# Kernel tuning notes

Measured on AMD Instinct MI355X. Metric: run time of the kernel, lower is better.

The kernel has to match this reference:

```python
import jax, jax.numpy as jnp
import numpy as np


def setup_inputs() -> dict:
    key = jax.random.key(0)
    k1, k2, k3 = jax.random.split(key, 3)
    N, M, H = 32768, 4096, 768
    fact = jax.random.normal(k1, (N, H), dtype=jnp.float32)
    elements_p = jax.random.normal(k2, (M, H), dtype=jnp.float32)
    # kaiming_uniform with a=sqrt(5) on [H,H]: bound = sqrt(6/((1+5)*H)) = 1/sqrt(H)
    bound = 1.0 / np.sqrt(H)
    weights = jax.random.uniform(k3, (H, H), dtype=jnp.float32, minval=-bound, maxval=bound)
    return {"fact": fact, "elements_p": elements_p, "weights": weights}


def reference(fact, elements_p, weights):
    # fact: [N,H], elements_p: [M,H], weights: [H,H]
    fact_Q = jnp.max(fact, axis=0, keepdims=True)                 # [1,H]
    f2e = (fact_Q @ weights) @ elements_p.T                        # [1,M]
    f2e = jax.nn.softmax(f2e, axis=-1)
    elements_p_ = jnp.sum(elements_p * f2e.T, axis=0, keepdims=True)  # [1,H]
    e2f = (fact @ weights) @ elements_p_.T                         # [N,1]
    e2f = jax.nn.softmax(e2f, axis=0)
    fact_ = jnp.sum(fact * e2f, axis=0, keepdims=True)             # [1,H]
    return (fact_, elements_p_)
```

## Files before the change

### kernel.cpp

```cpp
#include <hip/hip_runtime.h>
#include <math.h>


#define H 768
#define H4 192
#define PSTRIDE 772
#define ACC_OFF 4
#define NBLK 256
#define NQ 48
#define NCOL 192

__device__ __forceinline__ float wave_max(float x) {
#pragma unroll
  for (int o = 32; o; o >>= 1) x = fmaxf(x, __shfl_xor(x, o, 64));
  return x;
}
__device__ __forceinline__ float wave_sum(float x) {
#pragma unroll
  for (int o = 32; o; o >>= 1) x += __shfl_xor(x, o, 64);
  return x;
}
__device__ __forceinline__ float4 f4max(float4 a, float4 b) {
  return make_float4(fmaxf(a.x, b.x), fmaxf(a.y, b.y), fmaxf(a.z, b.z), fmaxf(a.w, b.w));
}

struct SMem {
  float4 sacc[8][H4];
  float sred[16];
};

__device__ __forceinline__ void stream_pass(const float4* __restrict__ X4,
                                            const float* __restrict__ wvec,
                                            float* __restrict__ part, int R,
                                            SMem& sm) {
  const int tid = threadIdx.x, lane = tid & 63, wv = tid >> 6;
  float4 wr[3];
#pragma unroll
  for (int j = 0; j < 3; ++j) wr[j] = ((const float4*)wvec)[lane + 64 * j];
  const int nw = NBLK * 8;
  const int gw = blockIdx.x * 8 + wv;
  const int rpw = (R + nw - 1) / nw;
  const int r0 = gw * rpw;
  const int r1 = min(R, r0 + rpw);
  float mrun = -INFINITY, l = 0.f;
  float4 acc[3];
#pragma unroll
  for (int j = 0; j < 3; ++j) acc[j] = make_float4(0.f, 0.f, 0.f, 0.f);
  for (int r = r0; r < r1; ++r) {
    const float4* row = X4 + (size_t)r * H4;
    float4 x[3];
    float s = 0.f;
#pragma unroll
    for (int j = 0; j < 3; ++j) {
      x[j] = row[lane + 64 * j];
      s = fmaf(x[j].x, wr[j].x, s);
      s = fmaf(x[j].y, wr[j].y, s);
      s = fmaf(x[j].z, wr[j].z, s);
      s = fmaf(x[j].w, wr[j].w, s);
    }
    s = wave_sum(s);
    const float mn = fmaxf(mrun, s);
    const float esc = __expf(mrun - mn);
    const float p = __expf(s - mn);
    l = fmaf(l, esc, p);
#pragma unroll
    for (int j = 0; j < 3; ++j) {
      acc[j].x = fmaf(acc[j].x, esc, p * x[j].x);
      acc[j].y = fmaf(acc[j].y, esc, p * x[j].y);
      acc[j].z = fmaf(acc[j].z, esc, p * x[j].z);
      acc[j].w = fmaf(acc[j].w, esc, p * x[j].w);
    }
    mrun = mn;
  }
  if (lane == 0) { sm.sred[wv] = mrun; sm.sred[8 + wv] = l; }
#pragma unroll
  for (int j = 0; j < 3; ++j) sm.sacc[wv][lane + 64 * j] = acc[j];
  __syncthreads();
  if (wv == 0) {
    float gm = -INFINITY;
#pragma unroll
    for (int w2 = 0; w2 < 8; ++w2) gm = fmaxf(gm, sm.sred[w2]);
    float fa[8];
    float L = 0.f;
#pragma unroll
    for (int w2 = 0; w2 < 8; ++w2) {
      const float lw = sm.sred[8 + w2];
      fa[w2] = (lw > 0.f) ? __expf(sm.sred[w2] - gm) : 0.f;
      L = fmaf(fa[w2], lw, L);
    }
    float* pb = part + (size_t)blockIdx.x * PSTRIDE;
#pragma unroll
    for (int j = 0; j < 3; ++j) {
      float4 a = make_float4(0.f, 0.f, 0.f, 0.f);
#pragma unroll
      for (int w2 = 0; w2 < 8; ++w2) {
        const float4 t = sm.sacc[w2][lane + 64 * j];
        a.x = fmaf(fa[w2], t.x, a.x);
        a.y = fmaf(fa[w2], t.y, a.y);
        a.z = fmaf(fa[w2], t.z, a.z);
        a.w = fmaf(fa[w2], t.w, a.w);
      }
      *(float4*)(pb + ACC_OFF + 4 * (lane + 64 * j)) = a;
    }
    if (lane == 0) { pb[0] = gm; pb[1] = L; }
  }
}

__global__ __launch_bounds__(192) void k_colmax(const float4* __restrict__ x4,
                                                float4* __restrict__ pmax4, int N,
                                                unsigned int* __restrict__ cnts,
                                                float* __restrict__ q,
                                                float* __restrict__ v) {
  const int t = threadIdx.x;
  if (blockIdx.x == 0) {
    if (t < 8) cnts[t] = 0u;
#pragma unroll
    for (int j = 0; j < 4; ++j) { q[t + 192 * j] = 0.f; v[t + 192 * j] = 0.f; }
  }
  const int rpb = (N + NBLK - 1) / NBLK;
  const int n0 = blockIdx.x * rpb;
  const int n1 = min(N, n0 + rpb);
  float4 m = make_float4(-INFINITY, -INFINITY, -INFINITY, -INFINITY);
#pragma unroll 8
  for (int n = n0; n < n1; ++n) m = f4max(m, x4[(size_t)n * H4 + t]);
  pmax4[(size_t)blockIdx.x * H4 + t] = m;
}

__global__ __launch_bounds__(192) void k_q(const float4* __restrict__ W4,
                                           const float* __restrict__ pmax,
                                           float* __restrict__ q) {
  const int tid = threadIdx.x;
  const int k0 = blockIdx.x * 16;
  __shared__ float sA[12][16];
  __shared__ float fQl[16];
  {
    const int col = tid & 15;
    const int grp = tid >> 4;
    float m = -INFINITY;
    for (int p = grp; p < NBLK; p += 12) m = fmaxf(m, pmax[(size_t)p * H + k0 + col]);
    sA[grp][col] = m;
    __syncthreads();
    if (tid < 16) {
      float mm = sA[0][tid];
#pragma unroll
      for (int g = 1; g < 12; ++g) mm = fmaxf(mm, sA[g][tid]);
      fQl[tid] = mm;
    }
    __syncthreads();
  }
  float4 acc = make_float4(0.f, 0.f, 0.f, 0.f);
#pragma unroll 4
  for (int kk = 0; kk < 16; ++kk) {
    const float f = fQl[kk];
    const float4 w = W4[(size_t)(k0 + kk) * H4 + tid];
    acc.x = fmaf(f, w.x, acc.x);
    acc.y = fmaf(f, w.y, acc.y);
    acc.z = fmaf(f, w.z, acc.z);
    acc.w = fmaf(f, w.w, acc.w);
  }
  atomicAdd(&q[4 * tid + 0], acc.x);
  atomicAdd(&q[4 * tid + 1], acc.y);
  atomicAdd(&q[4 * tid + 2], acc.z);
  atomicAdd(&q[4 * tid + 3], acc.w);
}

__global__ __launch_bounds__(512) void k_ep(const float4* __restrict__ ep4,
                                            const float* __restrict__ q,
                                            float* __restrict__ pm, int M) {
  __shared__ SMem sm;
  stream_pass(ep4, q, pm, M, sm);
}

__global__ __launch_bounds__(512) void k_epcomb_v(const float* __restrict__ P,
                                                  const float4* __restrict__ W4,
                                                  float4* __restrict__ out_ep,
                                                  float* __restrict__ v) {
  const int tid = threadIdx.x, lane = tid & 63, wv = tid >> 6;
  const int c = blockIdx.x;
  __shared__ float sred[16];
  __shared__ float4 swv[8];
  __shared__ float4 sr4;
  float m = -INFINITY, Lb = 0.f;
  float4 a = make_float4(0.f, 0.f, 0.f, 0.f);
  if (tid < NBLK) {
    const float* pb = P + (size_t)tid * PSTRIDE;
    m = pb[0];
    Lb = pb[1];
    a = *(const float4*)(pb + ACC_OFF + 4 * c);
  }
  float gm = wave_max(m);
  if (lane == 0) sred[wv] = gm;
  __syncthreads();
  gm = sred[0];
#pragma unroll
  for (int w2 = 1; w2 < 8; ++w2) gm = fmaxf(gm, sred[w2]);
  __syncthreads();
  const float e = (Lb > 0.f) ? __expf(m - gm) : 0.f;
  float L = e * Lb;
  a.x *= e; a.y *= e; a.z *= e; a.w *= e;
  L = wave_sum(L);
  a.x = wave_sum(a.x); a.y = wave_sum(a.y);
  a.z = wave_sum(a.z); a.w = wave_sum(a.w);
  if (lane == 0) { sred[8 + wv] = L; swv[wv] = a; }
  __syncthreads();
  if (tid == 0) {
    float Lt = 0.f;
    float4 s = make_float4(0.f, 0.f, 0.f, 0.f);
#pragma unroll
    for (int w2 = 0; w2 < 8; ++w2) {
      Lt += sred[8 + w2];
      const float4 t = swv[w2];
      s.x += t.x; s.y += t.y; s.z += t.z; s.w += t.w;
    }
    const float inv = 1.f / Lt;
    const float4 r = make_float4(s.x * inv, s.y * inv, s.z * inv, s.w * inv);
    out_ep[c] = r;
    sr4 = r;
  }
  __syncthreads();
  const float4 r4 = sr4;
  for (int i = tid; i < H; i += 512) {
    const float4 w = W4[(size_t)i * H4 + c];
    const float s = fmaf(w.x, r4.x, fmaf(w.y, r4.y, fmaf(w.z, r4.z, w.w * r4.w)));
    atomicAdd(&v[i], s);
  }
}

__global__ __launch_bounds__(512) void k_fact(const float4* __restrict__ X4,
                                              const float* __restrict__ v,
                                              float* __restrict__ pn,
                                              float* __restrict__ pn2, int R,
                                              unsigned int* __restrict__ cntA,
                                              unsigned int* __restrict__ cntB,
                                              float* __restrict__ outp) {
  const int tid = threadIdx.x, lane = tid & 63, wv = tid >> 6;
  __shared__ SMem sm;
  stream_pass(X4, v, pn, R, sm);

  __shared__ unsigned int s_rank;
  __syncthreads();
  if (tid == 0) {
    __threadfence();
    s_rank = atomicAdd(cntA, 1u);
  }
  __syncthreads();
  const unsigned int rank = s_rank;
  if (rank < (unsigned)(NBLK - 8)) return;

  if (tid == 0) {
    while (__hip_atomic_load(cntA, __ATOMIC_ACQUIRE, __HIP_MEMORY_SCOPE_AGENT) <
           (unsigned)NBLK)
      __builtin_amdgcn_s_sleep(8);
  }
  __syncthreads();
  __threadfence();

  const int slice = (int)rank - (NBLK - 8);
  const float* Pb = pn + (size_t)slice * 32 * PSTRIDE;
  __shared__ float s32m[32], s32l[32];
  if (tid < 32) {
    s32m[tid] = Pb[(size_t)tid * PSTRIDE];
    s32l[tid] = Pb[(size_t)tid * PSTRIDE + 1];
  }
  __syncthreads();
  float gms = -INFINITY;
#pragma unroll
  for (int b = 0; b < 32; ++b) gms = fmaxf(gms, s32m[b]);
  float4 a[3];
#pragma unroll
  for (int j = 0; j < 3; ++j) a[j] = make_float4(0.f, 0.f, 0.f, 0.f);
  for (int b = wv; b < 32; b += 8) {
    const float e = (s32l[b] > 0.f) ? __expf(s32m[b] - gms) : 0.f;
    const float4* pa = (const float4*)(Pb + (size_t)b * PSTRIDE + ACC_OFF);
#pragma unroll
    for (int j = 0; j < 3; ++j) {
      const float4 t = pa[lane + 64 * j];
      a[j].x = fmaf(e, t.x, a[j].x);
      a[j].y = fmaf(e, t.y, a[j].y);
      a[j].z = fmaf(e, t.z, a[j].z);
      a[j].w = fmaf(e, t.w, a[j].w);
    }
  }
  float lc = 0.f;
  if (tid < 32) lc = ((s32l[tid] > 0.f) ? __expf(s32m[tid] - gms) : 0.f) * s32l[tid];
  lc = wave_sum(lc);
  __syncthreads();
#pragma unroll
  for (int j = 0; j < 3; ++j) sm.sacc[wv][lane + 64 * j] = a[j];
  if (tid == 0) sm.sred[0] = lc;
  __syncthreads();
  float* qb = pn2 + (size_t)slice * PSTRIDE;
  if (tid < H4) {
    float4 s = sm.sacc[0][tid];
#pragma unroll
    for (int w2 = 1; w2 < 8; ++w2) {
      const float4 t = sm.sacc[w2][tid];
      s.x += t.x; s.y += t.y; s.z += t.z; s.w += t.w;
    }
    *(float4*)(qb + ACC_OFF + 4 * tid) = s;
  }
  if (tid == 0) { qb[0] = gms; qb[1] = sm.sred[0]; }

  __syncthreads();
  __shared__ unsigned int s_r2;
  if (tid == 0) {
    __threadfence();
    s_r2 = atomicAdd(cntB, 1u);
  }
  __syncthreads();
  if (s_r2 != 7u) return;
  __threadfence();

  __shared__ float s8m[8], s8l[8];
  if (tid < 8) {
    s8m[tid] = pn2[(size_t)tid * PSTRIDE];
    s8l[tid] = pn2[(size_t)tid * PSTRIDE + 1];
  }
  __syncthreads();
  float gm = -INFINITY;
#pragma unroll
  for (int k = 0; k < 8; ++k) gm = fmaxf(gm, s8m[k]);
  float Lt = 0.f;
#pragma unroll
  for (int k = 0; k < 8; ++k)
    Lt += ((s8l[k] > 0.f) ? __expf(s8m[k] - gm) : 0.f) * s8l[k];
  float4 b[3];
  {
    const int k = wv;
    const float e = (s8l[k] > 0.f) ? __expf(s8m[k] - gm) : 0.f;
    const float4* pa = (const float4*)(pn2 + (size_t)k * PSTRIDE + ACC_OFF);
#pragma unroll
    for (int j = 0; j < 3; ++j) {
      const float4 t = pa[lane + 64 * j];
      b[j] = make_float4(e * t.x, e * t.y, e * t.z, e * t.w);
    }
  }
  __syncthreads();
#pragma unroll
  for (int j = 0; j < 3; ++j) sm.sacc[wv][lane + 64 * j] = b[j];
  __syncthreads();
  if (tid < H4) {
    float4 s = sm.sacc[0][tid];
#pragma unroll
    for (int w2 = 1; w2 < 8; ++w2) {
      const float4 t = sm.sacc[w2][tid];
      s.x += t.x; s.y += t.y; s.z += t.z; s.w += t.w;
    }
    const float inv = 1.f / Lt;
    ((float4*)outp)[tid] = make_float4(s.x * inv, s.y * inv, s.z * inv, s.w * inv);
  }
}

extern "C" void kernel_launch(void* const* d_in, const int* in_sizes, int n_in,
                              void* d_out, int out_size, void* d_ws, size_t ws_size,
                              hipStream_t stream) {
  const float4* fact4 = (const float4*)d_in[0];
  const float4* ep4   = (const float4*)d_in[1];
  const float4* W4    = (const float4*)d_in[2];
  float* out = (float*)d_out;
  const int N = in_sizes[0] / H;
  const int M = in_sizes[1] / H;

  float* wsf = (float*)d_ws;
  unsigned int* cnts = (unsigned int*)d_ws;
  float* q     = wsf + 8;
  float* v     = wsf + 776;
  float* pmaxf = wsf + 1544;
  float* pm    = wsf + 198152;
  float* pn    = wsf + 395784;
  float* pn2   = wsf + 593416;

  k_colmax<<<NBLK, 192, 0, stream>>>(fact4, (float4*)pmaxf, N, cnts, q, v);
  k_q<<<NQ, 192, 0, stream>>>(W4, pmaxf, q);
  k_ep<<<NBLK, 512, 0, stream>>>(ep4, q, pm, M);
  k_epcomb_v<<<NCOL, 512, 0, stream>>>(pm, W4, (float4*)(out + H), v);
  k_fact<<<NBLK, 512, 0, stream>>>(fact4, v, pn, pn2, N, cnts + 0, cnts + 1, out);
}
```

Before: 222.2 us.

## Fuse colmax with q and ep pass with combine using last-block tails

Merges five launches into three. The column-max kernel now computes fact_Q @ W in its last 8 blocks, which spin on per-block flags. The elements pass now does the softmax combine and the W·r product in the last 8 blocks to arrive, selected by an atomic ticket counter. It also touches W early to warm the cache, and the combine step handles 24 columns per block instead of one column per block. This removes launch gaps and the tiny separate kernels. The cost is spin-waiting that assumes all blocks are co-resident. The MAGIC flags are never reset, so on later calls the tail blocks may not wait and could read stale partial maxima.

Measured after the change: 258.6 us. 1.16x slower.

```diff
diff --git a/kernel.cpp b/kernel.cpp
--- a/kernel.cpp
+++ b/kernel.cpp
@@ -7,8 +7,9 @@
 #define PSTRIDE 772
 #define ACC_OFF 4
 #define NBLK 256
-#define NQ 48
-#define NCOL 192
+#define NTAIL 8
+#define TAILB (NBLK - NTAIL)
+#define MAGIC 0xA5C3E917u
 
 __device__ __forceinline__ float wave_max(float x) {
 #pragma unroll
@@ -106,122 +107,191 @@
   }
 }
 
-__global__ __launch_bounds__(192) void k_colmax(const float4* __restrict__ x4,
-                                                float4* __restrict__ pmax4, int N,
-                                                unsigned int* __restrict__ cnts,
-                                                float* __restrict__ q,
-                                                float* __restrict__ v) {
+__global__ __launch_bounds__(192) void k_colmax_q(
+    const float4* __restrict__ x4, float4* __restrict__ pmax4, int N,
+    unsigned int* __restrict__ cnts, float* __restrict__ q,
+    float* __restrict__ v, const float4* __restrict__ W4,
+    unsigned int* __restrict__ flags) {
   const int t = threadIdx.x;
-  if (blockIdx.x == 0) {
+  const int b = blockIdx.x;
+  if (b == 0) {
     if (t < 8) cnts[t] = 0u;
 #pragma unroll
     for (int j = 0; j < 4; ++j) { q[t + 192 * j] = 0.f; v[t + 192 * j] = 0.f; }
   }
+  {
+    float d = 0.f;
+    const int base = b * 576;
+#pragma unroll
+    for (int j = 0; j < 3; ++j) {
+      const float4 w = W4[base + t + 192 * j];
+      d += w.x + w.y + w.z + w.w;
+    }
+    asm volatile("" ::"v"(d));
+  }
   const int rpb = (N + NBLK - 1) / NBLK;
-  const int n0 = blockIdx.x * rpb;
+  const int n0 = b * rpb;
   const int n1 = min(N, n0 + rpb);
   float4 m = make_float4(-INFINITY, -INFINITY, -INFINITY, -INFINITY);
 #pragma unroll 8
   for (int n = n0; n < n1; ++n) m = f4max(m, x4[(size_t)n * H4 + t]);
-  pmax4[(size_t)blockIdx.x * H4 + t] = m;
-}
-
-__global__ __launch_bounds__(192) void k_q(const float4* __restrict__ W4,
-                                           const float* __restrict__ pmax,
-                                           float* __restrict__ q) {
-  const int tid = threadIdx.x;
-  const int k0 = blockIdx.x * 16;
-  __shared__ float sA[12][16];
-  __shared__ float fQl[16];
+  pmax4[(size_t)b * H4 + t] = m;
+
+  __syncthreads();
+  if (t == 0) {
+    __threadfence();
+    __hip_atomic_store(&flags[b], MAGIC, __ATOMIC_RELEASE, __HIP_MEMORY_SCOPE_AGENT);
+  }
+  if (b < TAILB) return;
+
   {
-    const int col = tid & 15;
-    const int grp = tid >> 4;
-    float m = -INFINITY;
-    for (int p = grp; p < NBLK; p += 12) m = fmaxf(m, pmax[(size_t)p * H + k0 + col]);
-    sA[grp][col] = m;
-    __syncthreads();
-    if (tid < 16) {
-      float mm = sA[0][tid];
-#pragma unroll
-      for (int g = 1; g < 12; ++g) mm = fmaxf(mm, sA[g][tid]);
-      fQl[tid] = mm;
-    }
-    __syncthreads();
-  }
+    int ok = 1;
+    do {
+      ok = 1;
+      if (t < 64) {
+        ok = (__hip_atomic_load(&flags[t], __ATOMIC_ACQUIRE, __HIP_MEMORY_SCOPE_AGENT) == MAGIC) &&
+             (__hip_atomic_load(&flags[t + 64], __ATOMIC_ACQUIRE, __HIP_MEMORY_SCOPE_AGENT) == MAGIC) &&
+             (__hip_atomic_load(&flags[t + 128], __ATOMIC_ACQUIRE, __HIP_MEMORY_SCOPE_AGENT) == MAGIC) &&
+             (__hip_atomic_load(&flags[t + 192], __ATOMIC_ACQUIRE, __HIP_MEMORY_SCOPE_AGENT) == MAGIC);
+      }
+      if (__syncthreads_and(ok)) break;
+      __builtin_amdgcn_s_sleep(8);
+    } while (true);
+    __threadfence();
+  }
+
+  const int sl = b - TAILB;
+  const int k0 = sl * 96;
+  const float* pmaxf = (const float*)pmax4;
+  __shared__ float sfq2[2][96];
+  __shared__ float sfQ[96];
+  {
+    const int col = t % 96;
+    const int pg = t / 96;
+    float mm[8];
+#pragma unroll
+    for (int u = 0; u < 8; ++u) mm[u] = -INFINITY;
+    for (int i = 0; i < 128; i += 8) {
+#pragma unroll
+      for (int u = 0; u < 8; ++u) {
+        const int p = pg + 2 * (i + u);
+        mm[u] = fmaxf(mm[u], pmaxf[(size_t)p * H + k0 + col]);
+      }
+    }
+    float mr = mm[0];
+#pragma unroll
+    for (int u = 1; u < 8; ++u) mr = fmaxf(mr, mm[u]);
+    sfq2[pg][col] = mr;
+  }
+  __syncthreads();
+  if (t < 96) sfQ[t] = fmaxf(sfq2[0][t], sfq2[1][t]);
+  __syncthreads();
   float4 acc = make_float4(0.f, 0.f, 0.f, 0.f);
 #pragma unroll 4
-  for (int kk = 0; kk < 16; ++kk) {
-    const float f = fQl[kk];
-    const float4 w = W4[(size_t)(k0 + kk) * H4 + tid];
+  for (int kk = 0; kk < 96; ++kk) {
+    const float f = sfQ[kk];
+    const float4 w = W4[(size_t)(k0 + kk) * H4 + t];
     acc.x = fmaf(f, w.x, acc.x);
     acc.y = fmaf(f, w.y, acc.y);
     acc.z = fmaf(f, w.z, acc.z);
     acc.w = fmaf(f, w.w, acc.w);
   }
-  atomicAdd(&q[4 * tid + 0], acc.x);
-  atomicAdd(&q[4 * tid + 1], acc.y);
-  atomicAdd(&q[4 * tid + 2], acc.z);
-  atomicAdd(&q[4 * tid + 3], acc.w);
-}
-
-__global__ __launch_bounds__(512) void k_ep(const float4* __restrict__ ep4,
-                                            const float* __restrict__ q,
-                                            float* __restrict__ pm, int M) {
+  atomicAdd(&q[4 * t + 0], acc.x);
+  atomicAdd(&q[4 * t + 1], acc.y);
+  atomicAdd(&q[4 * t + 2], acc.z);
+  atomicAdd(&q[4 * t + 3], acc.w);
+}
+
+__global__ __launch_bounds__(512) void k_ep_comb(
+    const float4* __restrict__ ep4, const float* __restrict__ q,
+    float* __restrict__ pm, int M, const float4* __restrict__ W4,
+    float4* __restrict__ out_ep, float* __restrict__ v,
+    unsigned int* __restrict__ cnt) {
+  const int tid = threadIdx.x;
   __shared__ SMem sm;
   stream_pass(ep4, q, pm, M, sm);
-}
-
-__global__ __launch_bounds__(512) void k_epcomb_v(const float* __restrict__ P,
-                                                  const float4* __restrict__ W4,
-                                                  float4* __restrict__ out_ep,
-                                                  float* __restrict__ v) {
-  const int tid = threadIdx.x, lane = tid & 63, wv = tid >> 6;
-  const int c = blockIdx.x;
-  __shared__ float sred[16];
-  __shared__ float4 swv[8];
-  __shared__ float4 sr4;
-  float m = -INFINITY, Lb = 0.f;
-  float4 a = make_float4(0.f, 0.f, 0.f, 0.f);
+
+  __shared__ unsigned int s_rank;
+  __syncthreads();
+  if (tid == 0) {
+    __threadfence();
+    s_rank = atomicAdd(cnt, 1u);
+  }
+  __syncthreads();
+  const unsigned int rank = s_rank;
+  if (rank < (unsigned)TAILB) return;
+  if (tid == 0) {
+    while (__hip_atomic_load(cnt, __ATOMIC_ACQUIRE, __HIP_MEMORY_SCOPE_AGENT) <
+           (unsigned)NBLK)
+      __builtin_amdgcn_s_sleep(8);
+  }
+  __syncthreads();
+  __threadfence();
+
+  const int sl = (int)rank - TAILB;
+  const int cb4 = sl * 24;
+  const float* P = pm;
+  __shared__ float tm[NBLK], tl[NBLK], te[NBLK];
+  __shared__ float sgm, sLt4[4];
+  __shared__ float4 sga[21][24];
+  __shared__ float4 srr[24];
   if (tid < NBLK) {
     const float* pb = P + (size_t)tid * PSTRIDE;
-    m = pb[0];
-    Lb = pb[1];
-    a = *(const float4*)(pb + ACC_OFF + 4 * c);
-  }
-  float gm = wave_max(m);
-  if (lane == 0) sred[wv] = gm;
-  __syncthreads();
-  gm = sred[0];
-#pragma unroll
-  for (int w2 = 1; w2 < 8; ++w2) gm = fmaxf(gm, sred[w2]);
-  __syncthreads();
-  const float e = (Lb > 0.f) ? __expf(m - gm) : 0.f;
-  float L = e * Lb;
-  a.x *= e; a.y *= e; a.z *= e; a.w *= e;
-  L = wave_sum(L);
-  a.x = wave_sum(a.x); a.y = wave_sum(a.y);
-  a.z = wave_sum(a.z); a.w = wave_sum(a.w);
-  if (lane == 0) { sred[8 + wv] = L; swv[wv] = a; }
-  __syncthreads();
-  if (tid == 0) {
-    float Lt = 0.f;
-    float4 s = make_float4(0.f, 0.f, 0.f, 0.f);
-#pragma unroll
-    for (int w2 = 0; w2 < 8; ++w2) {
-      Lt += sred[8 + w2];
-      const float4 t = swv[w2];
-      s.x += t.x; s.y += t.y; s.z += t.z; s.w += t.w;
-    }
-    const float inv = 1.f / Lt;
+    tm[tid] = pb[0];
+    tl[tid] = pb[1];
+  }
+  __syncthreads();
+  if (tid < 64) {
+    float g = fmaxf(fmaxf(tm[tid], tm[tid + 64]), fmaxf(tm[tid + 128], tm[tid + 192]));
+    g = wave_max(g);
+    if (tid == 0) sgm = g;
+  }
+  __syncthreads();
+  const float gm = sgm;
+  if (tid < NBLK) te[tid] = (tl[tid] > 0.f) ? __expf(tm[tid] - gm) : 0.f;
+  __syncthreads();
+  if (tid < NBLK) {
+    float x = te[tid] * tl[tid];
+    x = wave_sum(x);
+    if ((tid & 63) == 0) sLt4[tid >> 6] = x;
+  }
+  __syncthreads();
+  const float inv = 1.f / (sLt4[0] + sLt4[1] + sLt4[2] + sLt4[3]);
+  if (tid < 504) {
+    const int c = tid % 24;
+    const int pg = tid / 24;
+    float4 a = make_float4(0.f, 0.f, 0.f, 0.f);
+    for (int p = pg; p < NBLK; p += 21) {
+      const float e = te[p];
+      const float4 t4 = *(const float4*)(P + (size_t)p * PSTRIDE + ACC_OFF + 4 * (cb4 + c));
+      a.x = fmaf(e, t4.x, a.x);
+      a.y = fmaf(e, t4.y, a.y);
+      a.z = fmaf(e, t4.z, a.z);
+      a.w = fmaf(e, t4.w, a.w);
+    }
+    sga[pg][c] = a;
+  }
+  __syncthreads();
+  if (tid < 24) {
+    float4 s = sga[0][tid];
+#pragma unroll
+    for (int pg = 1; pg < 21; ++pg) {
+      const float4 t4 = sga[pg][tid];
+      s.x += t4.x; s.y += t4.y; s.z += t4.z; s.w += t4.w;
+    }
     const float4 r = make_float4(s.x * inv, s.y * inv, s.z * inv, s.w * inv);
-    out_ep[c] = r;
-    sr4 = r;
-  }
-  __syncthreads();
-  const float4 r4 = sr4;
+    out_ep[cb4 + tid] = r;
+    srr[tid] = r;
+  }
+  __syncthreads();
   for (int i = tid; i < H; i += 512) {
-    const float4 w = W4[(size_t)i * H4 + c];
-    const float s = fmaf(w.x, r4.x, fmaf(w.y, r4.y, fmaf(w.z, r4.z, w.w * r4.w)));
+    float s = 0.f;
+#pragma unroll
+    for (int c = 0; c < 24; ++c) {
+      const float4 w = W4[(size_t)i * H4 + cb4 + c];
+      const float4 r = srr[c];
+      s = fmaf(w.x, r.x, fmaf(w.y, r.y, fmaf(w.z, r.z, fmaf(w.w, r.w, s))));
+    }
     atomicAdd(&v[i], s);
   }
 }
@@ -369,10 +439,9 @@
   float* pm    = wsf + 198152;
   float* pn    = wsf + 395784;
   float* pn2   = wsf + 593416;
-
-  k_colmax<<<NBLK, 192, 0, stream>>>(fact4, (float4*)pmaxf, N, cnts, q, v);
-  k_q<<<NQ, 192, 0, stream>>>(W4, pmaxf, q);
-  k_ep<<<NBLK, 512, 0, stream>>>(ep4, q, pm, M);
-  k_epcomb_v<<<NCOL, 512, 0, stream>>>(pm, W4, (float4*)(out + H), v);
-  k_fact<<<NBLK, 512, 0, stream>>>(fact4, v, pn, pn2, N, cnts + 0, cnts + 1, out);
-}
+  unsigned int* flags = (unsigned int*)(wsf + 599592);
+
+  k_colmax_q<<<NBLK, 192, 0, stream>>>(fact4, (float4*)pmaxf, N, cnts, q, v, W4, flags);
+  k_ep_comb<<<NBLK, 512, 0, stream>>>(ep4, q, pm, M, W4, (float4*)(out + H), v, cnts + 1);
+  k_fact<<<NBLK, 512, 0, stream>>>(fact4, v, pn, pn2, N, cnts + 2, cnts + 3, out);
+}
```
